# Performance work log

Hardware: AMD Instinct MI355X
Metric: run time of the kernel (lower is better)

## Reference

```python
import jax, jax.numpy as jnp
import numpy as np

HIDDEN = 128
HEADS = 8
HEAD_DIM = HIDDEN // HEADS
N_BLOCKS = 2048
N_EDGES = 4096


def setup_inputs() -> dict:
    key = jax.random.key(0)
    ks = jax.random.split(key, 14)
    s = 0.02
    return {
        "block_features": jax.random.normal(ks[0], (N_BLOCKS, HIDDEN), dtype=jnp.float32),
        "edge_indices": jax.random.randint(ks[1], (2, N_EDGES), 0, N_BLOCKS, dtype=jnp.int32),
        # edge_encoder: Linear(2H->H), ReLU, Linear(H->H)
        "W_e1": jax.random.normal(ks[2], (2 * HIDDEN, HIDDEN), dtype=jnp.float32) * s,
        "b_e1": jnp.zeros((HIDDEN,), dtype=jnp.float32),
        "W_e2": jax.random.normal(ks[3], (HIDDEN, HIDDEN), dtype=jnp.float32) * s,
        "b_e2": jnp.zeros((HIDDEN,), dtype=jnp.float32),
        "Wq": jax.random.normal(ks[4], (HIDDEN, HIDDEN), dtype=jnp.float32) * s,
        "bq": jnp.zeros((HIDDEN,), dtype=jnp.float32),
        "Wk": jax.random.normal(ks[5], (HIDDEN, HIDDEN), dtype=jnp.float32) * s,
        "bk": jnp.zeros((HIDDEN,), dtype=jnp.float32),
        "Wv": jax.random.normal(ks[6], (HIDDEN, HIDDEN), dtype=jnp.float32) * s,
        "bv": jnp.zeros((HIDDEN,), dtype=jnp.float32),
        "Wo": jax.random.normal(ks[7], (HIDDEN, HIDDEN), dtype=jnp.float32) * s,
        "bo": jnp.zeros((HIDDEN,), dtype=jnp.float32),
    }


def reference(block_features, edge_indices, W_e1, b_e1, W_e2, b_e2,
              Wq, bq, Wk, bk, Wv, bv, Wo, bo):
    n_blocks = block_features.shape[0]
    src_idx, dst_idx = edge_indices[0], edge_indices[1]

    # gather src/dst node features, concat -> edge MLP (dropout is identity in eval)
    ef = jnp.concatenate([block_features[src_idx], block_features[dst_idx]], axis=1)  # [E, 2H]
    ef = jnp.maximum(ef @ W_e1 + b_e1, 0.0) @ W_e2 + b_e2  # [E, H]

    E = ef.shape[0]
    scale = HEAD_DIM ** -0.5
    q = (ef @ Wq + bq).reshape(E, HEADS, HEAD_DIM)
    k = (ef @ Wk + bk).reshape(E, HEADS, HEAD_DIM)
    v = (ef @ Wv + bv).reshape(E, HEADS, HEAD_DIM)

    # dense attention over all edges
    scores = jnp.einsum("ehd,fhd->hef", q, k) * scale  # [H, E, E]
    attn = jax.nn.softmax(scores, axis=-1)
    attn_out = jnp.einsum("hef,fhd->ehd", attn, v).reshape(E, HIDDEN)
    updated_edges = attn_out @ Wo + bo  # [E, H]

    # scatter_sum back to destination nodes
    block_updates = jax.ops.segment_sum(updated_edges, dst_idx, num_segments=n_blocks)
    return block_features + block_updates
```

## Files before the change

### kernel.cpp

```cpp
#include <hip/hip_runtime.h>
#include <hip/hip_bf16.h>

#define NB 2048
#define NE 4096
#define HID 128
#define NHEAD 8
#define HD 16

#define QSCALE 0.36067376022224085f

typedef short s16x8 __attribute__((ext_vector_type(8)));
typedef float f32x4  __attribute__((ext_vector_type(4)));
typedef float f32x16 __attribute__((ext_vector_type(16)));

static __device__ __forceinline__ ushort f2bf(float x) {
    uint u = __builtin_bit_cast(uint, x);
    uint r = (u + 0x7fffu + ((u >> 16) & 1u)) >> 16;
    return (ushort)r;
}
static __device__ __forceinline__ uint pack2bf(float a, float b) {
    return (uint)f2bf(a) | ((uint)f2bf(b) << 16);
}
static __device__ __forceinline__ uint packrd(float a, float b) {
    uint ua = __builtin_bit_cast(uint, a) + 0x8000u;
    uint ub = __builtin_bit_cast(uint, b) + 0x8000u;
    return __builtin_amdgcn_perm(ub, ua, 0x07060302u);
}

__global__ __launch_bounds__(256) void convert_kernel(
    const float* __restrict__ We1, const float* __restrict__ We2,
    const float* __restrict__ Wq,  const float* __restrict__ Wk,
    const float* __restrict__ Wv,  const float* __restrict__ Wo,
    ushort* __restrict__ wb)
{
    int i = blockIdx.x * 256 + threadIdx.x;
    if (i < 8192) {
        int k = i >> 5, n4 = (i & 31) * 4;
        float4 t = *(const float4*)(We1 + k * HID + n4);
        wb[(n4 + 0) * 256 + k] = f2bf(t.x);
        wb[(n4 + 1) * 256 + k] = f2bf(t.y);
        wb[(n4 + 2) * 256 + k] = f2bf(t.z);
        wb[(n4 + 3) * 256 + k] = f2bf(t.w);
    } else if (i < 28672) {
        int j = i - 8192;
        int m = j >> 12;
        int r = j & 4095;
        int k = r >> 5, n4 = (r & 31) * 4;
        const float* W = (m == 0) ? We2 : (m == 1) ? Wq : (m == 2) ? Wk
                       : (m == 3) ? Wv : Wo;
        float4 t = *(const float4*)(W + k * HID + n4);
        ushort* o = wb + 32768 + m * 16384;
        o[(n4 + 0) * 128 + k] = f2bf(t.x);
        o[(n4 + 1) * 128 + k] = f2bf(t.y);
        o[(n4 + 2) * 128 + k] = f2bf(t.z);
        o[(n4 + 3) * 128 + k] = f2bf(t.w);
    }
}

__global__ __launch_bounds__(512, 2) void mlp_qkv_kernel(
    const float* __restrict__ bf, const int* __restrict__ src, const int* __restrict__ dst,
    const ushort* __restrict__ wb,
    const float* __restrict__ be1, const float* __restrict__ be2,
    const float* __restrict__ bq,  const float* __restrict__ bk, const float* __restrict__ bv,
    ushort* __restrict__ qg, ushort* __restrict__ kg, ushort* __restrict__ vT,
    float4* __restrict__ out_init)
{
    __shared__ ushort sX[16][264];
    __shared__ ushort sH[16][136];
    __shared__ ushort sE[16][136];

    const int tid = threadIdx.x;
    const int w   = tid >> 6;
    const int l   = tid & 63;
    const int lo16 = l & 15;
    const int hi4  = l >> 4;
    const int e0 = blockIdx.x * 16;

    if (tid < 256)
        out_init[blockIdx.x * 256 + tid] = ((const float4*)bf)[blockIdx.x * 256 + tid];

    const ushort* We1T = wb;
    const ushort* We2T = wb + 32768;
    const ushort* WqT  = wb + 49152;
    const ushort* WkT  = wb + 65536;
    const ushort* WvT  = wb + 81920;

    s16x8 B1[8], B2[4], BQ[4], BK[4], BV[4];
    #pragma unroll
    for (int k0 = 0; k0 < 8; k0++)
        B1[k0] = *(const s16x8*)(We1T + (w * 16 + lo16) * 256 + k0 * 32 + hi4 * 8);
    #pragma unroll
    for (int k0 = 0; k0 < 4; k0++) {
        B2[k0] = *(const s16x8*)(We2T + (w * 16 + lo16) * 128 + k0 * 32 + hi4 * 8);
        BQ[k0] = *(const s16x8*)(WqT  + (w * 16 + lo16) * 128 + k0 * 32 + hi4 * 8);
        BK[k0] = *(const s16x8*)(WkT  + (w * 16 + lo16) * 128 + k0 * 32 + hi4 * 8);
        BV[k0] = *(const s16x8*)(WvT  + (w * 16 + lo16) * 128 + k0 * 32 + hi4 * 8);
    }
    const float bias1 = be1[w * 16 + lo16];
    const float bias2 = be2[w * 16 + lo16];
    const float biasq = bq[w * 16 + lo16];
    const float biask = bk[w * 16 + lo16];
    const float biasv = bv[w * 16 + lo16];

    {
        const int r  = tid >> 5;
        const int sg = tid & 31;
        const int e  = e0 + r;
        const int node = (sg < 16) ? src[e] : dst[e];
        const float4* rowp = (const float4*)(bf + node * HID);
        const int fb = (sg & 15) * 2;
        float4 t0 = rowp[fb], t1 = rowp[fb + 1];
        *(uint2*)&sX[r][sg * 8]     = make_uint2(pack2bf(t0.x, t0.y), pack2bf(t0.z, t0.w));
        *(uint2*)&sX[r][sg * 8 + 4] = make_uint2(pack2bf(t1.x, t1.y), pack2bf(t1.z, t1.w));
    }
    __syncthreads();

    f32x4 acc;

    {
        acc = (f32x4){bias1, bias1, bias1, bias1};
        #pragma unroll
        for (int k0 = 0; k0 < 8; k0++) {
            s16x8 a = *(const s16x8*)&sX[lo16][k0 * 32 + hi4 * 8];
            acc = __builtin_amdgcn_mfma_f32_16x16x32_bf16(a, B1[k0], acc, 0, 0, 0);
        }
        #pragma unroll
        for (int r = 0; r < 4; r++)
            sH[hi4 * 4 + r][w * 16 + lo16] = f2bf(fmaxf(acc[r], 0.0f));
    }
    __syncthreads();

    {
        acc = (f32x4){bias2, bias2, bias2, bias2};
        #pragma unroll
        for (int k0 = 0; k0 < 4; k0++) {
            s16x8 a = *(const s16x8*)&sH[lo16][k0 * 32 + hi4 * 8];
            acc = __builtin_amdgcn_mfma_f32_16x16x32_bf16(a, B2[k0], acc, 0, 0, 0);
        }
        #pragma unroll
        for (int r = 0; r < 4; r++)
            sE[hi4 * 4 + r][w * 16 + lo16] = f2bf(acc[r]);
    }
    __syncthreads();

#define PROJ(BARR, BIAS, STORE) do { \
    acc = (f32x4){BIAS, BIAS, BIAS, BIAS}; \
    _Pragma("unroll") \
    for (int k0 = 0; k0 < 4; k0++) { \
        s16x8 a = *(const s16x8*)&sE[lo16][k0 * 32 + hi4 * 8]; \
        acc = __builtin_amdgcn_mfma_f32_16x16x32_bf16(a, BARR[k0], acc, 0, 0, 0); \
    } \
    _Pragma("unroll") \
    for (int r = 0; r < 4; r++) { STORE; } \
} while (0)

    PROJ(BQ, biasq, { int e = e0 + hi4 * 4 + r;
                      qg[(w * NE + e) * 16 + lo16] = f2bf(acc[r] * QSCALE); });
    PROJ(BK, biask, { int e = e0 + hi4 * 4 + r;
                      kg[(w * NE + e) * 16 + lo16] = f2bf(acc[r]); });
    PROJ(BV, biasv, { int e = e0 + hi4 * 4 + r;
                      vT[(w * 16 + lo16) * NE + e] = f2bf(acc[r]); });
#undef PROJ
}

__global__ __launch_bounds__(512) void attn_kernel(
    const ushort* __restrict__ qg, const ushort* __restrict__ kg,
    const ushort* __restrict__ vT, ushort* __restrict__ Og)
{
    __shared__ ushort Pbuf[8][2048];

    const int tid = threadIdx.x;
    const int w   = tid >> 6;
    const int l   = tid & 63;
    const int h   = blockIdx.y;
    const int q0  = blockIdx.x * 32;
    const int lo16 = l & 15, hi4 = l >> 4;
    const int lo32 = l & 31, hi2 = l >> 5;

    ushort* Pw = &Pbuf[w][0];

    const s16x8 qf = *(const s16x8*)(qg + (h * NE + q0 + lo32) * 16 + hi2 * 8);
    const s16x8 ones = __builtin_bit_cast(s16x8,
        make_uint4(0x3f803f80u, 0x3f803f80u, 0x3f803f80u, 0x3f803f80u));

    const f32x16 z16 = {};
    f32x4 o0 = {0,0,0,0}, o1 = {0,0,0,0};
    f32x4 l0 = {0,0,0,0}, l1 = {0,0,0,0};

    const int kbase = w * (NE / 8);
    const ushort* kp = kg + (size_t)h * NE * 16;
    const ushort* vp = vT + (size_t)(h * 16 + lo16) * NE;

    s16x8 kf = *(const s16x8*)(kp + (kbase + lo32) * 16 + hi2 * 8);
    s16x8 vf = *(const s16x8*)(vp + kbase + hi4 * 8);

    #pragma unroll 2
    for (int kt = 0; kt < 16; kt++) {
        const s16x8 kc = kf, vc = vf;
        const int key1 = kbase + ((kt + 1) & 15) * 32;
        kf = *(const s16x8*)(kp + (key1 + lo32) * 16 + hi2 * 8);
        vf = *(const s16x8*)(vp + key1 + hi4 * 8);

        f32x16 s = __builtin_amdgcn_mfma_f32_32x32x16_bf16(kc, qf, z16, 0, 0, 0);

        const int b8 = (kt & 1) * 8;
        #pragma unroll
        for (int g = 0; g < 4; g++) {
            uint2 w2 = make_uint2(
                packrd(__builtin_amdgcn_exp2f(s[4*g]),   __builtin_amdgcn_exp2f(s[4*g+1])),
                packrd(__builtin_amdgcn_exp2f(s[4*g+2]), __builtin_amdgcn_exp2f(s[4*g+3])));
            *(uint2*)&Pw[((b8 + 2*g + hi2) * 32 + lo32) * 4] = w2;
        }

        uint2 alo = *(const uint2*)&Pw[((b8 + 2*hi4)     * 32 + lo16) * 4];
        uint2 ahi = *(const uint2*)&Pw[((b8 + 2*hi4 + 1) * 32 + lo16) * 4];
        uint2 blo = *(const uint2*)&Pw[((b8 + 2*hi4)     * 32 + 16 + lo16) * 4];
        uint2 bhi = *(const uint2*)&Pw[((b8 + 2*hi4 + 1) * 32 + 16 + lo16) * 4];
        s16x8 pb0 = __builtin_bit_cast(s16x8, make_uint4(alo.x, alo.y, ahi.x, ahi.y));
        s16x8 pb1 = __builtin_bit_cast(s16x8, make_uint4(blo.x, blo.y, bhi.x, bhi.y));

        o0 = __builtin_amdgcn_mfma_f32_16x16x32_bf16(vc, pb0, o0, 0, 0, 0);
        o1 = __builtin_amdgcn_mfma_f32_16x16x32_bf16(vc, pb1, o1, 0, 0, 0);
        l0 = __builtin_amdgcn_mfma_f32_16x16x32_bf16(ones, pb0, l0, 0, 0, 0);
        l1 = __builtin_amdgcn_mfma_f32_16x16x32_bf16(ones, pb1, l1, 0, 0, 0);
    }

    __syncthreads();
    float* sO = (float*)&Pbuf[0][0];
    #pragma unroll
    for (int r = 0; r < 4; r++) {
        sO[(w * 32 + lo16) * 18 + hi4 * 4 + r]      = o0[r];
        sO[(w * 32 + 16 + lo16) * 18 + hi4 * 4 + r] = o1[r];
    }
    if (hi4 == 0) {
        sO[(w * 32 + lo16) * 18 + 16]      = l0[0];
        sO[(w * 32 + 16 + lo16) * 18 + 16] = l1[0];
    }
    __syncthreads();

    {
        const int q = tid >> 4;
        const int d = tid & 15;
        float sum = 0.0f, Lq = 0.0f;
        #pragma unroll
        for (int ww = 0; ww < 8; ww++) {
            sum += sO[(ww * 32 + q) * 18 + d];
            Lq  += sO[(ww * 32 + q) * 18 + 16];
        }
        Og[(q0 + q) * HID + h * 16 + d] = f2bf(sum / Lq);
    }
}

__global__ __launch_bounds__(512, 2) void wo_scatter_kernel(
    const ushort* __restrict__ Og, const ushort* __restrict__ wb,
    const float* __restrict__ bo, const int* __restrict__ dst,
    float* __restrict__ out)
{
    const int tid = threadIdx.x;
    const int w   = tid >> 6;
    const int l   = tid & 63;
    const int lo16 = l & 15, hi4 = l >> 4;
    const int e0 = blockIdx.x * 16;
    const ushort* WoT = wb + 98304;

    s16x8 BO[4], AO[4];
    #pragma unroll
    for (int k0 = 0; k0 < 4; k0++) {
        BO[k0] = *(const s16x8*)(WoT + (w * 16 + lo16) * 128 + k0 * 32 + hi4 * 8);
        AO[k0] = *(const s16x8*)(Og + (e0 + lo16) * HID + k0 * 32 + hi4 * 8);
    }
    int dste[4];
    #pragma unroll
    for (int r = 0; r < 4; r++) dste[r] = dst[e0 + hi4 * 4 + r];
    const float b_ = bo[w * 16 + lo16];

    f32x4 acc = (f32x4){b_, b_, b_, b_};
    #pragma unroll
    for (int k0 = 0; k0 < 4; k0++)
        acc = __builtin_amdgcn_mfma_f32_16x16x32_bf16(AO[k0], BO[k0], acc, 0, 0, 0);

    #pragma unroll
    for (int r = 0; r < 4; r++) {
        atomicAdd(out + dste[r] * HID + w * 16 + lo16, acc[r]);
    }
}

extern "C" void kernel_launch(void* const* d_in, const int* in_sizes, int n_in,
                              void* d_out, int out_size, void* d_ws, size_t ws_size,
                              hipStream_t stream)
{
    const float* bf  = (const float*)d_in[0];
    const int*   ei  = (const int*)d_in[1];
    const int*   src = ei;
    const int*   dst = ei + NE;
    const float* We1 = (const float*)d_in[2];
    const float* be1 = (const float*)d_in[3];
    const float* We2 = (const float*)d_in[4];
    const float* be2 = (const float*)d_in[5];
    const float* Wq  = (const float*)d_in[6];
    const float* bq  = (const float*)d_in[7];
    const float* Wk  = (const float*)d_in[8];
    const float* bk  = (const float*)d_in[9];
    const float* Wv  = (const float*)d_in[10];
    const float* bv  = (const float*)d_in[11];
    const float* Wo  = (const float*)d_in[12];
    const float* bo  = (const float*)d_in[13];

    char* ws = (char*)d_ws;
    ushort* wb  = (ushort*)(ws);
    ushort* qg  = (ushort*)(ws + (1u<<18));
    ushort* kg  = (ushort*)(ws + (1u<<18) + (1u<<20));
    ushort* vT  = (ushort*)(ws + (1u<<18) + (2u<<20));
    ushort* Og  = (ushort*)(ws + (1u<<18) + (3u<<20));

    convert_kernel<<<112, 256, 0, stream>>>(We1, We2, Wq, Wk, Wv, Wo, wb);
    mlp_qkv_kernel<<<NE / 16, 512, 0, stream>>>(bf, src, dst, wb, be1, be2, bq, bk, bv,
                                                qg, kg, vT, (float4*)d_out);
    attn_kernel<<<dim3(NE / 32, NHEAD), 512, 0, stream>>>(qg, kg, vT, Og);
    wo_scatter_kernel<<<NE / 16, 512, 0, stream>>>(Og, wb, bo, dst, (float*)d_out);
}
```

Before: 50.65 us.

## Fold softmax row-sum into PV MFMA via padded V with ones row

V is stored transposed into a 32-row-per-head buffer whose padding rows are pre-filled, with row 16 set to ones and the rest zero, so a single 32x32x16 MFMA computes both P·V and the softmax denominator. This replaces four 16x16 MFMAs per tile, two of which multiplied by a constant ones vector. Register prefetching of K/V is dropped in favour of direct loads, and launch bounds are raised so more blocks can be resident per CU. In exchange, the V buffer doubles in size and the convert kernel does extra fill writes on every call.

```diff
diff --git a/kernel.cpp b/kernel.cpp
--- a/kernel.cpp
+++ b/kernel.cpp
@@ -31,9 +31,14 @@
     const float* __restrict__ We1, const float* __restrict__ We2,
     const float* __restrict__ Wq,  const float* __restrict__ Wk,
     const float* __restrict__ Wv,  const float* __restrict__ Wo,
-    ushort* __restrict__ wb)
+    ushort* __restrict__ wb, uint4* __restrict__ vfill)
 {
     int i = blockIdx.x * 256 + threadIdx.x;
+    {
+        int h = i >> 13, rr = (i >> 9) & 15, c = i & 511;
+        uint v = (rr == 0) ? 0x3f803f80u : 0u;
+        vfill[(h * 32 + 16 + rr) * 512 + c] = make_uint4(v, v, v, v);
+    }
     if (i < 8192) {
         int k = i >> 5, n4 = (i & 31) * 4;
         float4 t = *(const float4*)(We1 + k * HID + n4);
@@ -62,7 +67,7 @@
     const ushort* __restrict__ wb,
     const float* __restrict__ be1, const float* __restrict__ be2,
     const float* __restrict__ bq,  const float* __restrict__ bk, const float* __restrict__ bv,
-    ushort* __restrict__ qg, ushort* __restrict__ kg, ushort* __restrict__ vT,
+    ushort* __restrict__ qg, ushort* __restrict__ kg, ushort* __restrict__ vTx,
     float4* __restrict__ out_init)
 {
     __shared__ ushort sX[16][264];
@@ -159,13 +164,13 @@
     PROJ(BK, biask, { int e = e0 + hi4 * 4 + r;
                       kg[(w * NE + e) * 16 + lo16] = f2bf(acc[r]); });
     PROJ(BV, biasv, { int e = e0 + hi4 * 4 + r;
-                      vT[(w * 16 + lo16) * NE + e] = f2bf(acc[r]); });
+                      vTx[(w * 32 + lo16) * NE + e] = f2bf(acc[r]); });
 #undef PROJ
 }
 
-__global__ __launch_bounds__(512) void attn_kernel(
+__global__ __launch_bounds__(512, 8) void attn_kernel(
     const ushort* __restrict__ qg, const ushort* __restrict__ kg,
-    const ushort* __restrict__ vT, ushort* __restrict__ Og)
+    const ushort* __restrict__ vTx, ushort* __restrict__ Og)
 {
     __shared__ ushort Pbuf[8][2048];
 
@@ -174,34 +179,26 @@
     const int l   = tid & 63;
     const int h   = blockIdx.y;
     const int q0  = blockIdx.x * 32;
-    const int lo16 = l & 15, hi4 = l >> 4;
     const int lo32 = l & 31, hi2 = l >> 5;
 
     ushort* Pw = &Pbuf[w][0];
 
     const s16x8 qf = *(const s16x8*)(qg + (h * NE + q0 + lo32) * 16 + hi2 * 8);
-    const s16x8 ones = __builtin_bit_cast(s16x8,
-        make_uint4(0x3f803f80u, 0x3f803f80u, 0x3f803f80u, 0x3f803f80u));
-
-    const f32x16 z16 = {};
-    f32x4 o0 = {0,0,0,0}, o1 = {0,0,0,0};
-    f32x4 l0 = {0,0,0,0}, l1 = {0,0,0,0};
-
+
+    f32x16 accO = {};
     const int kbase = w * (NE / 8);
     const ushort* kp = kg + (size_t)h * NE * 16;
-    const ushort* vp = vT + (size_t)(h * 16 + lo16) * NE;
-
-    s16x8 kf = *(const s16x8*)(kp + (kbase + lo32) * 16 + hi2 * 8);
-    s16x8 vf = *(const s16x8*)(vp + kbase + hi4 * 8);
+    const ushort* vp = vTx + (size_t)(h * 32 + lo32) * NE;
 
     #pragma unroll 2
     for (int kt = 0; kt < 16; kt++) {
-        const s16x8 kc = kf, vc = vf;
-        const int key1 = kbase + ((kt + 1) & 15) * 32;
-        kf = *(const s16x8*)(kp + (key1 + lo32) * 16 + hi2 * 8);
-        vf = *(const s16x8*)(vp + key1 + hi4 * 8);
-
-        f32x16 s = __builtin_amdgcn_mfma_f32_32x32x16_bf16(kc, qf, z16, 0, 0, 0);
+        const int key0 = kbase + kt * 32;
+        s16x8 kc  = *(const s16x8*)(kp + (key0 + lo32) * 16 + hi2 * 8);
+        s16x8 va0 = *(const s16x8*)(vp + key0 + hi2 * 8);
+        s16x8 va1 = *(const s16x8*)(vp + key0 + 16 + hi2 * 8);
+
+        f32x16 s = {};
+        s = __builtin_amdgcn_mfma_f32_32x32x16_bf16(kc, qf, s, 0, 0, 0);
 
         const int b8 = (kt & 1) * 8;
         #pragma unroll
@@ -212,29 +209,33 @@
             *(uint2*)&Pw[((b8 + 2*g + hi2) * 32 + lo32) * 4] = w2;
         }
 
-        uint2 alo = *(const uint2*)&Pw[((b8 + 2*hi4)     * 32 + lo16) * 4];
-        uint2 ahi = *(const uint2*)&Pw[((b8 + 2*hi4 + 1) * 32 + lo16) * 4];
-        uint2 blo = *(const uint2*)&Pw[((b8 + 2*hi4)     * 32 + 16 + lo16) * 4];
-        uint2 bhi = *(const uint2*)&Pw[((b8 + 2*hi4 + 1) * 32 + 16 + lo16) * 4];
-        s16x8 pb0 = __builtin_bit_cast(s16x8, make_uint4(alo.x, alo.y, ahi.x, ahi.y));
-        s16x8 pb1 = __builtin_bit_cast(s16x8, make_uint4(blo.x, blo.y, bhi.x, bhi.y));
-
-        o0 = __builtin_amdgcn_mfma_f32_16x16x32_bf16(vc, pb0, o0, 0, 0, 0);
-        o1 = __builtin_amdgcn_mfma_f32_16x16x32_bf16(vc, pb1, o1, 0, 0, 0);
-        l0 = __builtin_amdgcn_mfma_f32_16x16x32_bf16(ones, pb0, l0, 0, 0, 0);
-        l1 = __builtin_amdgcn_mfma_f32_16x16x32_bf16(ones, pb1, l1, 0, 0, 0);
+        uint2 c0 = *(const uint2*)&Pw[((b8 + 2*hi2)     * 32 + lo32) * 4];
+        uint2 c1 = *(const uint2*)&Pw[((b8 + 2*hi2 + 1) * 32 + lo32) * 4];
+        uint2 c2 = *(const uint2*)&Pw[((b8 + 4 + 2*hi2)     * 32 + lo32) * 4];
+        uint2 c3 = *(const uint2*)&Pw[((b8 + 4 + 2*hi2 + 1) * 32 + lo32) * 4];
+        s16x8 pb0 = __builtin_bit_cast(s16x8, make_uint4(c0.x, c0.y, c1.x, c1.y));
+        s16x8 pb1 = __builtin_bit_cast(s16x8, make_uint4(c2.x, c2.y, c3.x, c3.y));
+
+        accO = __builtin_amdgcn_mfma_f32_32x32x16_bf16(va0, pb0, accO, 0, 0, 0);
+        accO = __builtin_amdgcn_mfma_f32_32x32x16_bf16(va1, pb1, accO, 0, 0, 0);
     }
 
     __syncthreads();
     float* sO = (float*)&Pbuf[0][0];
-    #pragma unroll
-    for (int r = 0; r < 4; r++) {
-        sO[(w * 32 + lo16) * 18 + hi4 * 4 + r]      = o0[r];
-        sO[(w * 32 + 16 + lo16) * 18 + hi4 * 4 + r] = o1[r];
-    }
-    if (hi4 == 0) {
-        sO[(w * 32 + lo16) * 18 + 16]      = l0[0];
-        sO[(w * 32 + 16 + lo16) * 18 + 16] = l1[0];
+    {
+        float* row = &sO[(w * 32 + lo32) * 18];
+        if (hi2 == 0) {
+            *(float2*)&row[0]  = make_float2(accO[0], accO[1]);
+            *(float2*)&row[2]  = make_float2(accO[2], accO[3]);
+            *(float2*)&row[8]  = make_float2(accO[4], accO[5]);
+            *(float2*)&row[10] = make_float2(accO[6], accO[7]);
+            row[16] = accO[8];
+        } else {
+            *(float2*)&row[4]  = make_float2(accO[0], accO[1]);
+            *(float2*)&row[6]  = make_float2(accO[2], accO[3]);
+            *(float2*)&row[12] = make_float2(accO[4], accO[5]);
+            *(float2*)&row[14] = make_float2(accO[6], accO[7]);
+        }
     }
     __syncthreads();
 
@@ -310,12 +311,12 @@
     ushort* wb  = (ushort*)(ws);
     ushort* qg  = (ushort*)(ws + (1u<<18));
     ushort* kg  = (ushort*)(ws + (1u<<18) + (1u<<20));
-    ushort* vT  = (ushort*)(ws + (1u<<18) + (2u<<20));
-    ushort* Og  = (ushort*)(ws + (1u<<18) + (3u<<20));
-
-    convert_kernel<<<112, 256, 0, stream>>>(We1, We2, Wq, Wk, Wv, Wo, wb);
+    ushort* vTx = (ushort*)(ws + (1u<<18) + (2u<<20));
+    ushort* Og  = (ushort*)(ws + (1u<<18) + (4u<<20));
+
+    convert_kernel<<<256, 256, 0, stream>>>(We1, We2, Wq, Wk, Wv, Wo, wb, (uint4*)vTx);
     mlp_qkv_kernel<<<NE / 16, 512, 0, stream>>>(bf, src, dst, wb, be1, be2, bq, bk, bv,
-                                                qg, kg, vT, (float4*)d_out);
-    attn_kernel<<<dim3(NE / 32, NHEAD), 512, 0, stream>>>(qg, kg, vT, Og);
+                                                qg, kg, vTx, (float4*)d_out);
+    attn_kernel<<<dim3(NE / 32, NHEAD), 512, 0, stream>>>(qg, kg, vTx, Og);
     wo_scatter_kernel<<<NE / 16, 512, 0, stream>>>(Og, wb, bo, dst, (float*)d_out);
 }
```

After: 60.55 us. +19.5%, slower.

## Compute softmax denominators with scalar sums and drop K/V prefetch in attention

Applied to the files above, without the earlier changes.

Replaces the two ones-vector MFMAs that accumulated row sums of P with per-lane fp32 accumulation of the exp values, combined by one cross-half shuffle. It removes the software prefetch of the next K/V tile and sets launch bounds to 8 waves-per-EU minimum to cut register pressure and raise occupancy. Row sums now come from unrounded fp32 exps rather than bf16-rounded P, which shifts normalization slightly. Load latency is no longer hidden by prefetch and must be covered by occupancy instead.

```diff
diff --git a/kernel.cpp b/kernel.cpp
--- a/kernel.cpp
+++ b/kernel.cpp
@@ -163,7 +163,7 @@
 #undef PROJ
 }
 
-__global__ __launch_bounds__(512) void attn_kernel(
+__global__ __launch_bounds__(512, 8) void attn_kernel(
     const ushort* __restrict__ qg, const ushort* __restrict__ kg,
     const ushort* __restrict__ vT, ushort* __restrict__ Og)
 {
@@ -180,35 +180,31 @@
     ushort* Pw = &Pbuf[w][0];
 
     const s16x8 qf = *(const s16x8*)(qg + (h * NE + q0 + lo32) * 16 + hi2 * 8);
-    const s16x8 ones = __builtin_bit_cast(s16x8,
-        make_uint4(0x3f803f80u, 0x3f803f80u, 0x3f803f80u, 0x3f803f80u));
 
     const f32x16 z16 = {};
     f32x4 o0 = {0,0,0,0}, o1 = {0,0,0,0};
-    f32x4 l0 = {0,0,0,0}, l1 = {0,0,0,0};
+    float L = 0.0f;
 
     const int kbase = w * (NE / 8);
     const ushort* kp = kg + (size_t)h * NE * 16;
     const ushort* vp = vT + (size_t)(h * 16 + lo16) * NE;
 
-    s16x8 kf = *(const s16x8*)(kp + (kbase + lo32) * 16 + hi2 * 8);
-    s16x8 vf = *(const s16x8*)(vp + kbase + hi4 * 8);
-
     #pragma unroll 2
     for (int kt = 0; kt < 16; kt++) {
-        const s16x8 kc = kf, vc = vf;
-        const int key1 = kbase + ((kt + 1) & 15) * 32;
-        kf = *(const s16x8*)(kp + (key1 + lo32) * 16 + hi2 * 8);
-        vf = *(const s16x8*)(vp + key1 + hi4 * 8);
+        const int key0 = kbase + kt * 32;
+        s16x8 kc = *(const s16x8*)(kp + (key0 + lo32) * 16 + hi2 * 8);
+        s16x8 vc = *(const s16x8*)(vp + key0 + hi4 * 8);
 
         f32x16 s = __builtin_amdgcn_mfma_f32_32x32x16_bf16(kc, qf, z16, 0, 0, 0);
 
+        float e[16];
+        #pragma unroll
+        for (int i = 0; i < 16; i++) { e[i] = __builtin_amdgcn_exp2f(s[i]); L += e[i]; }
+
         const int b8 = (kt & 1) * 8;
         #pragma unroll
         for (int g = 0; g < 4; g++) {
-            uint2 w2 = make_uint2(
-                packrd(__builtin_amdgcn_exp2f(s[4*g]),   __builtin_amdgcn_exp2f(s[4*g+1])),
-                packrd(__builtin_amdgcn_exp2f(s[4*g+2]), __builtin_amdgcn_exp2f(s[4*g+3])));
+            uint2 w2 = make_uint2(packrd(e[4*g], e[4*g+1]), packrd(e[4*g+2], e[4*g+3]));
             *(uint2*)&Pw[((b8 + 2*g + hi2) * 32 + lo32) * 4] = w2;
         }
 
@@ -221,9 +217,9 @@
 
         o0 = __builtin_amdgcn_mfma_f32_16x16x32_bf16(vc, pb0, o0, 0, 0, 0);
         o1 = __builtin_amdgcn_mfma_f32_16x16x32_bf16(vc, pb1, o1, 0, 0, 0);
-        l0 = __builtin_amdgcn_mfma_f32_16x16x32_bf16(ones, pb0, l0, 0, 0, 0);
-        l1 = __builtin_amdgcn_mfma_f32_16x16x32_bf16(ones, pb1, l1, 0, 0, 0);
-    }
+    }
+
+    float Lf = L + __shfl_xor(L, 32, 64);
 
     __syncthreads();
     float* sO = (float*)&Pbuf[0][0];
@@ -232,10 +228,7 @@
         sO[(w * 32 + lo16) * 18 + hi4 * 4 + r]      = o0[r];
         sO[(w * 32 + 16 + lo16) * 18 + hi4 * 4 + r] = o1[r];
     }
-    if (hi4 == 0) {
-        sO[(w * 32 + lo16) * 18 + 16]      = l0[0];
-        sO[(w * 32 + 16 + lo16) * 18 + 16] = l1[0];
-    }
+    if (hi2 == 0) sO[(w * 32 + lo32) * 18 + 16] = Lf;
     __syncthreads();
 
     {
```

After: 47.89 us, median of 2. 5.5% less time.
